# Kernel tuning notes

Measured on AMD Instinct MI355X. Metric: run time of the kernel, lower is better.

The kernel has to match this reference:

```python
import jax, jax.numpy as jnp
import numpy as np

EPS = 1e-5
HEADS = 4
DIM_HEAD = 64


def setup_inputs() -> dict:
    key = jax.random.key(0)
    k1, k2, k3, k4, k5, k6 = jax.random.split(key, 6)
    B, C, T, H, W = 2, 128, 40, 8, 8
    inner = HEADS * DIM_HEAD  # 256
    x = jax.random.normal(k1, (B, C, T, H, W), dtype=jnp.float32)
    g = jnp.ones((1, C, 1, 1, 1), dtype=jnp.float32) + 0.1 * jax.random.normal(k2, (1, C, 1, 1, 1), dtype=jnp.float32)
    b = 0.1 * jax.random.normal(k3, (1, C, 1, 1, 1), dtype=jnp.float32)
    w_qkv = 0.02 * jax.random.normal(k4, (inner * 3, C), dtype=jnp.float32)  # Conv1d(dim, inner*3, 1) weight squeezed
    w_out = 0.02 * jax.random.normal(k5, (C, inner), dtype=jnp.float32)      # Conv1d(inner, dim, 1) weight squeezed
    b_out = 0.02 * jax.random.normal(k6, (C,), dtype=jnp.float32)
    return {"x": x, "g": g, "b": b, "w_qkv": w_qkv, "w_out": w_out, "b_out": b_out}


def reference(x, g, b, w_qkv, w_out, b_out):
    B, C, T, H, W = x.shape
    n = T * H * W
    scale = DIM_HEAD ** -0.5
    # channel LayerNorm (var over dim=1, unbiased=False)
    mean = jnp.mean(x, axis=1, keepdims=True)
    std = jnp.sqrt(jnp.var(x, axis=1, keepdims=True))
    xn = (x - mean) / (std + EPS) * g + b
    xf = xn.reshape(B, C, n)  # b c n
    # 1x1 conv == matmul over channels
    qkv = jnp.einsum('oc,bcn->bon', w_qkv, xf)
    q, k, v = jnp.split(qkv, 3, axis=1)  # each [B, heads*d, n]
    def to_heads(t):  # b (h d) n -> b h n d
        return t.reshape(B, HEADS, DIM_HEAD, n).transpose(0, 1, 3, 2)
    q, k, v = to_heads(q) * scale, to_heads(k), to_heads(v)
    sim = jnp.einsum('bhid,bhjd->bhij', q, k)
    attn = jax.nn.softmax(sim, axis=-1)
    out = jnp.einsum('bhij,bhjd->bhid', attn, v)
    out = out.transpose(0, 1, 3, 2).reshape(B, HEADS * DIM_HEAD, n)  # b (h d) n
    out = jnp.einsum('oc,bcn->bon', w_out, out) + b_out[None, :, None]
    return out.reshape(B, C, T, H, W)
```

## Files before the change

kernel.cpp:

```cpp
#include <hip/hip_runtime.h>
#include <hip/hip_bf16.h>

#define HEADS 4
#define DHEAD 64
#define CC 128
#define NPOS 2560
#define NB 2
#define NSPLIT 4
#define NT_SPLIT ((NPOS / 64) / NSPLIT)

#define XN_ELE  ((size_t)NB * NPOS * CC)
#define QKV_ELE ((size_t)NB * HEADS * NPOS * DHEAD)
#define WS_BASE_BYTES  ((XN_ELE + 4 * QKV_ELE) * 2)
#define WS_SPLIT_BYTES ((XN_ELE + (4 + NSPLIT) * QKV_ELE) * 2 \
                        + (size_t)NSPLIT * NB * HEADS * NPOS * 8)

typedef __attribute__((ext_vector_type(8))) short short8;
typedef __attribute__((ext_vector_type(4))) short short4_t;
typedef __attribute__((ext_vector_type(4))) float f32x4;

#define SIDX(row, col) (((row) << 6) + ((col) ^ (((row) & 7) << 3)))

static __device__ __forceinline__ float b2f(short u) {
    union { unsigned int i; float f; } v;
    v.i = ((unsigned int)(unsigned short)u) << 16;
    return v.f;
}
static __device__ __forceinline__ short f2b(float f) {
    __hip_bfloat16 h = __float2bfloat16(f);
    union { __hip_bfloat16 h; unsigned short u; } v; v.h = h;
    return (short)v.u;
}

__global__ __launch_bounds__(256) void ln_kernel(
    const float* __restrict__ x, const float* __restrict__ g,
    const float* __restrict__ bb, short* __restrict__ xn) {
    int p0 = blockIdx.x * 64, b = blockIdx.y;
    __shared__ float tile[128][65];
    __shared__ float redsum[4][64], redsq[4][64], meanS[64], invS[64];
    int t = threadIdx.x, p = t & 63, cpart = t >> 6;
    float s = 0.f, sq = 0.f;
    for (int k = 0; k < 32; k++) {
        int c = cpart * 32 + k;
        float v = x[((b * CC + c) * NPOS) + p0 + p];
        tile[c][p] = v;
        s += v; sq += v * v;
    }
    redsum[cpart][p] = s; redsq[cpart][p] = sq;
    __syncthreads();
    if (t < 64) {
        float S = redsum[0][t] + redsum[1][t] + redsum[2][t] + redsum[3][t];
        float Q = redsq[0][t] + redsq[1][t] + redsq[2][t] + redsq[3][t];
        float mean = S * (1.f / CC);
        float var = fmaxf(Q * (1.f / CC) - mean * mean, 0.f);
        meanS[t] = mean;
        invS[t] = 1.f / (sqrtf(var) + 1e-5f);
    }
    __syncthreads();
    for (int k = 0; k < 32; k++) {
        int idx = k * 256 + t;
        int c = idx & 127, pp = idx >> 7;
        float v = (tile[c][pp] - meanS[pp]) * invS[pp] * g[c] + bb[c];
        xn[((size_t)(b * NPOS) + p0 + pp) * CC + c] = f2b(v);
    }
}

__global__ __launch_bounds__(256) void qkv_kernel(
    const float* __restrict__ w, const short* __restrict__ xn,
    short* __restrict__ q_ws, short* __restrict__ k_ws, short* __restrict__ v_ws) {
    int pt = blockIdx.x, ot = blockIdx.y, b = blockIdx.z;
    int p0 = pt * 64, o0 = ot * 64;
    __shared__ short Ws[64][136];
    __shared__ short Xs[64][136];
    int t = threadIdx.x, wv = t >> 6, l = t & 63;
    for (int i = 0; i < 8; i++) {
        int gidx = i * 256 + t;
        int r = gidx >> 5, cg = gidx & 31;
        f32x4 wv4 = *(const f32x4*)&w[(size_t)(o0 + r) * CC + cg * 4];
        short4_t sv = { f2b(wv4[0]), f2b(wv4[1]), f2b(wv4[2]), f2b(wv4[3]) };
        *(short4_t*)&Ws[r][cg * 4] = sv;
    }
    for (int i = 0; i < 4; i++) {
        int idx = i * 256 + t;
        int r = idx >> 4, ch = idx & 15;
        *(short8*)&Xs[r][ch * 8] = *(const short8*)&xn[((size_t)(b * NPOS) + p0 + r) * CC + ch * 8];
    }
    __syncthreads();
    f32x4 acc[4] = {{0,0,0,0},{0,0,0,0},{0,0,0,0},{0,0,0,0}};
    int lr = l & 15, lg = l >> 4;
    for (int kk = 0; kk < 4; kk++) {
        short8 a = *(short8*)&Ws[wv * 16 + lr][kk * 32 + lg * 8];
        for (int fb = 0; fb < 4; fb++) {
            short8 bf = *(short8*)&Xs[fb * 16 + lr][kk * 32 + lg * 8];
            acc[fb] = __builtin_amdgcn_mfma_f32_16x16x32_bf16(a, bf, acc[fb], 0, 0, 0);
        }
    }
    int orow0 = o0 + wv * 16 + lg * 4;
    int sec = orow0 >> 8;
    int oi = orow0 & 255, h = oi >> 6, d0 = oi & 63;
    size_t bh = (size_t)(b * HEADS + h);
    for (int fb = 0; fb < 4; fb++) {
        int pos = p0 + fb * 16 + lr;
        if (sec == 0) {
            short4_t qv = { f2b(acc[fb][0] * 0.125f), f2b(acc[fb][1] * 0.125f),
                            f2b(acc[fb][2] * 0.125f), f2b(acc[fb][3] * 0.125f) };
            *(short4_t*)&q_ws[(bh * NPOS + pos) * DHEAD + d0] = qv;
        } else if (sec == 1) {
            short4_t kv = { f2b(acc[fb][0]), f2b(acc[fb][1]), f2b(acc[fb][2]), f2b(acc[fb][3]) };
            *(short4_t*)&k_ws[(bh * NPOS + pos) * DHEAD + d0] = kv;
        } else {
            for (int r = 0; r < 4; r++)
                v_ws[(bh * DHEAD + d0 + r) * NPOS + pos] = f2b(acc[fb][r]);
        }
    }
}

template <int NT>
static __device__ __forceinline__ void attn_core(
    const short* __restrict__ kbp, const short* __restrict__ vbp,
    const short8* qreg, int kt0,
    short* Ks0, short* Ks1, short* Vs0, short* Vs1, short* PsT,
    int t, float& m_, float& l_, f32x4* acc) {
    int wv = t >> 6, l = t & 63;
    int lr = l & 15, lg = l >> 4;
    int sr0 = t >> 3, sr1 = sr0 + 32, sc = (t & 7) * 8;
    int prow = wv * 16 + lr;
    short* KsA[2] = { Ks0, Ks1 };
    short* VsA[2] = { Vs0, Vs1 };

    {
        int koff = kt0 * 64;
        *(short8*)&KsA[0][SIDX(sr0, sc)] = *(const short8*)&kbp[(size_t)(koff + sr0) * DHEAD + sc];
        *(short8*)&KsA[0][SIDX(sr1, sc)] = *(const short8*)&kbp[(size_t)(koff + sr1) * DHEAD + sc];
        *(short8*)&VsA[0][SIDX(sr0, sc)] = *(const short8*)&vbp[(size_t)sr0 * NPOS + koff + sc];
        *(short8*)&VsA[0][SIDX(sr1, sc)] = *(const short8*)&vbp[(size_t)sr1 * NPOS + koff + sc];
    }
    __syncthreads();

    for (int it = 0; it < NT; it++) {
        int cur = it & 1;
        bool pf = (it + 1 < NT);
        short8 kr0, kr1, vr0, vr1;
        if (pf) {
            int koff = (kt0 + it + 1) * 64;
            kr0 = *(const short8*)&kbp[(size_t)(koff + sr0) * DHEAD + sc];
            kr1 = *(const short8*)&kbp[(size_t)(koff + sr1) * DHEAD + sc];
            vr0 = *(const short8*)&vbp[(size_t)sr0 * NPOS + koff + sc];
            vr1 = *(const short8*)&vbp[(size_t)sr1 * NPOS + koff + sc];
        }
        f32x4 sf[4] = {{0,0,0,0},{0,0,0,0},{0,0,0,0},{0,0,0,0}};
        #pragma unroll
        for (int kk = 0; kk < 2; kk++) {
            #pragma unroll
            for (int fb = 0; fb < 4; fb++) {
                short8 kb = *(short8*)&KsA[cur][SIDX(fb * 16 + lr, kk * 32 + lg * 8)];
                sf[fb] = __builtin_amdgcn_mfma_f32_16x16x32_bf16(kb, qreg[kk], sf[fb], 0, 0, 0);
            }
        }
        float m0 = fmaxf(fmaxf(sf[0][0], sf[0][1]), fmaxf(sf[0][2], sf[0][3]));
        float m1 = fmaxf(fmaxf(sf[1][0], sf[1][1]), fmaxf(sf[1][2], sf[1][3]));
        float m2 = fmaxf(fmaxf(sf[2][0], sf[2][1]), fmaxf(sf[2][2], sf[2][3]));
        float m3 = fmaxf(fmaxf(sf[3][0], sf[3][1]), fmaxf(sf[3][2], sf[3][3]));
        float mx = fmaxf(fmaxf(m0, m1), fmaxf(m2, m3));
        mx = fmaxf(mx, __shfl_xor(mx, 16, 64));
        mx = fmaxf(mx, __shfl_xor(mx, 32, 64));
        float nm = fmaxf(m_, mx);
        float alpha = __expf(m_ - nm);
        float ps[4][4];
        float rs = 0.f;
        #pragma unroll
        for (int fb = 0; fb < 4; fb++) {
            float s0 = __expf(sf[fb][0] - nm), s1 = __expf(sf[fb][1] - nm);
            float s2 = __expf(sf[fb][2] - nm), s3 = __expf(sf[fb][3] - nm);
            ps[fb][0] = s0; ps[fb][1] = s1; ps[fb][2] = s2; ps[fb][3] = s3;
            rs += (s0 + s1) + (s2 + s3);
        }
        rs += __shfl_xor(rs, 16, 64);
        rs += __shfl_xor(rs, 32, 64);
        l_ = l_ * alpha + rs;
        m_ = nm;
        #pragma unroll
        for (int db = 0; db < 4; db++) {
            acc[db][0] *= alpha; acc[db][1] *= alpha;
            acc[db][2] *= alpha; acc[db][3] *= alpha;
        }
        #pragma unroll
        for (int fb = 0; fb < 4; fb++) {
            short4_t pk = { f2b(ps[fb][0]), f2b(ps[fb][1]), f2b(ps[fb][2]), f2b(ps[fb][3]) };
            *(short4_t*)&PsT[SIDX(prow, fb * 16 + lg * 4)] = pk;
        }
        #pragma unroll
        for (int kk = 0; kk < 2; kk++) {
            short8 pb = *(short8*)&PsT[SIDX(prow, kk * 32 + lg * 8)];
            #pragma unroll
            for (int db = 0; db < 4; db++) {
                short8 va = *(short8*)&VsA[cur][SIDX(db * 16 + lr, kk * 32 + lg * 8)];
                acc[db] = __builtin_amdgcn_mfma_f32_16x16x32_bf16(va, pb, acc[db], 0, 0, 0);
            }
        }
        if (pf) {
            *(short8*)&KsA[cur ^ 1][SIDX(sr0, sc)] = kr0;
            *(short8*)&KsA[cur ^ 1][SIDX(sr1, sc)] = kr1;
            *(short8*)&VsA[cur ^ 1][SIDX(sr0, sc)] = vr0;
            *(short8*)&VsA[cur ^ 1][SIDX(sr1, sc)] = vr1;
        }
        __syncthreads();
    }
}

__global__ __launch_bounds__(256) void attn_kernel(
    const short* __restrict__ q_ws, const short* __restrict__ k_ws,
    const short* __restrict__ v_ws, short* __restrict__ o_ws) {
    int qt = blockIdx.x, bh = blockIdx.y;
    int q0 = qt * 64;
    __shared__ short Ks[2][64 * 64];
    __shared__ short Vs[2][64 * 64];
    __shared__ short PsT[64 * 64];
    int t = threadIdx.x, wv = t >> 6, l = t & 63;
    int lr = l & 15, lg = l >> 4;
    const short* kbp = k_ws + (size_t)bh * NPOS * DHEAD;
    const short* vbp = v_ws + (size_t)bh * DHEAD * NPOS;
    short8 qreg[2];
    for (int kk = 0; kk < 2; kk++)
        qreg[kk] = *(const short8*)&q_ws[((size_t)bh * NPOS + q0 + wv * 16 + lr) * DHEAD + kk * 32 + lg * 8];
    float m_ = -1e9f, l_ = 0.f;
    f32x4 acc[4] = {{0,0,0,0},{0,0,0,0},{0,0,0,0},{0,0,0,0}};
    attn_core<NPOS / 64>(kbp, vbp, qreg, 0, Ks[0], Ks[1], Vs[0], Vs[1], PsT, t, m_, l_, acc);
    int h = bh & (HEADS - 1), b = bh >> 2;
    float inv = 1.f / l_;
    int pos = q0 + wv * 16 + lr;
    #pragma unroll
    for (int db = 0; db < 4; db++) {
        short4_t ov = { f2b(acc[db][0] * inv), f2b(acc[db][1] * inv),
                        f2b(acc[db][2] * inv), f2b(acc[db][3] * inv) };
        *(short4_t*)&o_ws[((size_t)(b * NPOS) + pos) * 256 + h * DHEAD + db * 16 + lg * 4] = ov;
    }
}

__global__ __launch_bounds__(256) void attn_split_kernel(
    const short* __restrict__ q_ws, const short* __restrict__ k_ws,
    const short* __restrict__ v_ws, short* __restrict__ po, float* __restrict__ ml) {
    int qt = blockIdx.x, bh = blockIdx.y, s = blockIdx.z;
    int q0 = qt * 64;
    __shared__ short Ks[2][64 * 64];
    __shared__ short Vs[2][64 * 64];
    __shared__ short PsT[64 * 64];
    int t = threadIdx.x, wv = t >> 6, l = t & 63;
    int lr = l & 15, lg = l >> 4;
    const short* kbp = k_ws + (size_t)bh * NPOS * DHEAD;
    const short* vbp = v_ws + (size_t)bh * DHEAD * NPOS;
    short8 qreg[2];
    for (int kk = 0; kk < 2; kk++)
        qreg[kk] = *(const short8*)&q_ws[((size_t)bh * NPOS + q0 + wv * 16 + lr) * DHEAD + kk * 32 + lg * 8];
    float m_ = -1e9f, l_ = 0.f;
    f32x4 acc[4] = {{0,0,0,0},{0,0,0,0},{0,0,0,0},{0,0,0,0}};
    attn_core<NT_SPLIT>(kbp, vbp, qreg, s * NT_SPLIT, Ks[0], Ks[1], Vs[0], Vs[1], PsT, t, m_, l_, acc);
    float inv = 1.f / l_;
    int pos = q0 + wv * 16 + lr;
    size_t sb = (size_t)(s * NB * HEADS + bh);
    #pragma unroll
    for (int db = 0; db < 4; db++) {
        short4_t ov = { f2b(acc[db][0] * inv), f2b(acc[db][1] * inv),
                        f2b(acc[db][2] * inv), f2b(acc[db][3] * inv) };
        *(short4_t*)&po[(sb * NPOS + pos) * DHEAD + db * 16 + lg * 4] = ov;
    }
    if (lg == 0) {
        ml[2 * (sb * NPOS + pos) + 0] = m_;
        ml[2 * (sb * NPOS + pos) + 1] = l_;
    }
}

__global__ __launch_bounds__(256) void combine_kernel(
    const short* __restrict__ po, const float* __restrict__ ml, short* __restrict__ o_ws) {
    int tid = blockIdx.x * 256 + threadIdx.x;
    int c8 = tid & 31;
    int posb = tid >> 5;
    int b = posb / NPOS, pos = posb - b * NPOS;
    int h = c8 >> 3, d0 = (c8 & 7) * 8;
    int bh = b * HEADS + h;
    float ms[NSPLIT], ls[NSPLIT], m = -1e30f;
    #pragma unroll
    for (int s = 0; s < NSPLIT; s++) {
        size_t sb = (size_t)(s * NB * HEADS + bh);
        ms[s] = ml[2 * (sb * NPOS + pos) + 0];
        ls[s] = ml[2 * (sb * NPOS + pos) + 1];
        m = fmaxf(m, ms[s]);
    }
    float w[NSPLIT], wsum = 0.f;
    #pragma unroll
    for (int s = 0; s < NSPLIT; s++) { w[s] = ls[s] * __expf(ms[s] - m); wsum += w[s]; }
    float o8[8] = {0,0,0,0,0,0,0,0};
    #pragma unroll
    for (int s = 0; s < NSPLIT; s++) {
        size_t sb = (size_t)(s * NB * HEADS + bh);
        short8 v = *(const short8*)&po[(sb * NPOS + pos) * DHEAD + d0];
        #pragma unroll
        for (int j = 0; j < 8; j++) o8[j] += w[s] * b2f(v[j]);
    }
    float inv = 1.f / wsum;
    short8 ov;
    #pragma unroll
    for (int j = 0; j < 8; j++) ov[j] = f2b(o8[j] * inv);
    *(short8*)&o_ws[((size_t)posb) * 256 + h * DHEAD + d0] = ov;
}

__global__ __launch_bounds__(256) void proj_kernel(
    const float* __restrict__ w_out, const float* __restrict__ b_out,
    const short* __restrict__ o_ws, float* __restrict__ out) {
    int pt = blockIdx.x, ct = blockIdx.y, b = blockIdx.z;
    int p0 = pt * 64, c0 = ct * 64;
    __shared__ short Ws[64][264];
    __shared__ short Os[64][264];
    int t = threadIdx.x, wv = t >> 6, l = t & 63;
    int lr = l & 15, lg = l >> 4;
    for (int i = 0; i < 16; i++) {
        int gidx = i * 256 + t;
        int r = gidx >> 6, cg = gidx & 63;
        f32x4 wv4 = *(const f32x4*)&w_out[(size_t)(c0 + r) * 256 + cg * 4];
        short4_t sv = { f2b(wv4[0]), f2b(wv4[1]), f2b(wv4[2]), f2b(wv4[3]) };
        *(short4_t*)&Ws[r][cg * 4] = sv;
    }
    for (int i = 0; i < 8; i++) {
        int gidx = i * 256 + t;
        int r = gidx >> 5, ch = gidx & 31;
        *(short8*)&Os[r][ch * 8] = *(const short8*)&o_ws[((size_t)(b * NPOS) + p0 + r) * 256 + ch * 8];
    }
    __syncthreads();
    f32x4 acc[4] = {{0,0,0,0},{0,0,0,0},{0,0,0,0},{0,0,0,0}};
    for (int kc = 0; kc < 8; kc++) {
        short8 a = *(short8*)&Ws[wv * 16 + lr][kc * 32 + lg * 8];
        #pragma unroll
        for (int fb = 0; fb < 4; fb++) {
            short8 ob = *(short8*)&Os[fb * 16 + lr][kc * 32 + lg * 8];
            acc[fb] = __builtin_amdgcn_mfma_f32_16x16x32_bf16(a, ob, acc[fb], 0, 0, 0);
        }
    }
    for (int r = 0; r < 4; r++) {
        int c = c0 + wv * 16 + lg * 4 + r;
        float bias = b_out[c];
        for (int fb = 0; fb < 4; fb++) {
            float vv = acc[fb][r] + bias;
            out[((size_t)(b * CC) + c) * NPOS + p0 + fb * 16 + lr] = vv;
        }
    }
}

extern "C" void kernel_launch(void* const* d_in, const int* in_sizes, int n_in,
                              void* d_out, int out_size, void* d_ws, size_t ws_size,
                              hipStream_t stream) {
    const float* x     = (const float*)d_in[0];
    const float* g     = (const float*)d_in[1];
    const float* b     = (const float*)d_in[2];
    const float* w_qkv = (const float*)d_in[3];
    const float* w_out = (const float*)d_in[4];
    const float* b_out = (const float*)d_in[5];
    float* out = (float*)d_out;

    const size_t out_bytes = (size_t)out_size * sizeof(float);

    {
        const int exp_sizes[6] = {655360, 128, 128, 98304, 32768, 128};
        int bad = -1;
        if (n_in != 6) bad = 15;
        else for (int i = 0; i < 6; i++) if (in_sizes[i] != exp_sizes[i]) { bad = i; break; }
        if (bad >= 0) { hipMemsetAsync(d_out, 0x50 | bad, out_bytes, stream); return; }
    }
    if (ws_size < WS_BASE_BYTES) {
        int mb = (int)(ws_size >> 20); if (mb > 15) mb = 15;
        hipMemsetAsync(d_out, 0x40 | mb, out_bytes, stream);
        return;
    }

    short* xn   = (short*)d_ws;
    short* q_ws = xn + XN_ELE;
    short* k_ws = q_ws + QKV_ELE;
    short* v_ws = k_ws + QKV_ELE;
    short* o_ws = v_ws + QKV_ELE;
    short* po   = o_ws + QKV_ELE;
    float* ml   = (float*)(po + NSPLIT * QKV_ELE);

    const bool use_split = (ws_size >= WS_SPLIT_BYTES);

    (void)hipGetLastError();
    ln_kernel<<<dim3(NPOS / 64, NB), 256, 0, stream>>>(x, g, b, xn);
    qkv_kernel<<<dim3(NPOS / 64, 12, NB), 256, 0, stream>>>(w_qkv, xn, q_ws, k_ws, v_ws);
    if (use_split) {
        attn_split_kernel<<<dim3(NPOS / 64, NB * HEADS, NSPLIT), 256, 0, stream>>>(q_ws, k_ws, v_ws, po, ml);
        combine_kernel<<<dim3(NB * NPOS * 32 / 256), 256, 0, stream>>>(po, ml, o_ws);
    } else {
        attn_kernel<<<dim3(NPOS / 64, NB * HEADS), 256, 0, stream>>>(q_ws, k_ws, v_ws, o_ws);
    }
    proj_kernel<<<dim3(NPOS / 64, 2, NB), 256, 0, stream>>>(w_out, b_out, o_ws, out);
    if (hipGetLastError() != hipSuccess) {
        hipMemsetAsync(d_out, 0xF0, out_bytes, stream);
    }
}
```

Measured before the change: 129.7 us.

## Fuse split-combine into projection, add lazy softmax rescale, single-buffer K/V

Removes the separate combine kernel and merges the split-KV reduction into the output projection's load stage, saving one launch and a round trip of the combined output through global memory. The softmax update now rescales the accumulators only when the running max rises by more than a threshold for some lane in the wave, which skips most alpha multiplies. K/V shared tiles go from double to single buffering, with an extra barrier around the refill. That cuts LDS use but serialises the tile store against compute. The proj blocks duplicate combine work across the two channel tiles.

```diff
diff --git a/kernel.cpp b/kernel.cpp
--- a/kernel.cpp
+++ b/kernel.cpp
@@ -119,26 +119,23 @@
 static __device__ __forceinline__ void attn_core(
     const short* __restrict__ kbp, const short* __restrict__ vbp,
     const short8* qreg, int kt0,
-    short* Ks0, short* Ks1, short* Vs0, short* Vs1, short* PsT,
+    short* Ks, short* Vs, short* PsT,
     int t, float& m_, float& l_, f32x4* acc) {
     int wv = t >> 6, l = t & 63;
     int lr = l & 15, lg = l >> 4;
     int sr0 = t >> 3, sr1 = sr0 + 32, sc = (t & 7) * 8;
     int prow = wv * 16 + lr;
-    short* KsA[2] = { Ks0, Ks1 };
-    short* VsA[2] = { Vs0, Vs1 };
 
     {
         int koff = kt0 * 64;
-        *(short8*)&KsA[0][SIDX(sr0, sc)] = *(const short8*)&kbp[(size_t)(koff + sr0) * DHEAD + sc];
-        *(short8*)&KsA[0][SIDX(sr1, sc)] = *(const short8*)&kbp[(size_t)(koff + sr1) * DHEAD + sc];
-        *(short8*)&VsA[0][SIDX(sr0, sc)] = *(const short8*)&vbp[(size_t)sr0 * NPOS + koff + sc];
-        *(short8*)&VsA[0][SIDX(sr1, sc)] = *(const short8*)&vbp[(size_t)sr1 * NPOS + koff + sc];
+        *(short8*)&Ks[SIDX(sr0, sc)] = *(const short8*)&kbp[(size_t)(koff + sr0) * DHEAD + sc];
+        *(short8*)&Ks[SIDX(sr1, sc)] = *(const short8*)&kbp[(size_t)(koff + sr1) * DHEAD + sc];
+        *(short8*)&Vs[SIDX(sr0, sc)] = *(const short8*)&vbp[(size_t)sr0 * NPOS + koff + sc];
+        *(short8*)&Vs[SIDX(sr1, sc)] = *(const short8*)&vbp[(size_t)sr1 * NPOS + koff + sc];
     }
     __syncthreads();
 
     for (int it = 0; it < NT; it++) {
-        int cur = it & 1;
         bool pf = (it + 1 < NT);
         short8 kr0, kr1, vr0, vr1;
         if (pf) {
@@ -153,7 +150,7 @@
         for (int kk = 0; kk < 2; kk++) {
             #pragma unroll
             for (int fb = 0; fb < 4; fb++) {
-                short8 kb = *(short8*)&KsA[cur][SIDX(fb * 16 + lr, kk * 32 + lg * 8)];
+                short8 kb = *(short8*)&Ks[SIDX(fb * 16 + lr, kk * 32 + lg * 8)];
                 sf[fb] = __builtin_amdgcn_mfma_f32_16x16x32_bf16(kb, qreg[kk], sf[fb], 0, 0, 0);
             }
         }
@@ -164,26 +161,29 @@
         float mx = fmaxf(fmaxf(m0, m1), fmaxf(m2, m3));
         mx = fmaxf(mx, __shfl_xor(mx, 16, 64));
         mx = fmaxf(mx, __shfl_xor(mx, 32, 64));
-        float nm = fmaxf(m_, mx);
-        float alpha = __expf(m_ - nm);
+        if (!__all(mx - m_ <= 8.0f)) {
+            float nm = fmaxf(m_, mx);
+            float alpha = __expf(m_ - nm);
+            l_ *= alpha;
+            #pragma unroll
+            for (int db = 0; db < 4; db++) {
+                acc[db][0] *= alpha; acc[db][1] *= alpha;
+                acc[db][2] *= alpha; acc[db][3] *= alpha;
+            }
+            m_ = nm;
+        }
         float ps[4][4];
         float rs = 0.f;
         #pragma unroll
         for (int fb = 0; fb < 4; fb++) {
-            float s0 = __expf(sf[fb][0] - nm), s1 = __expf(sf[fb][1] - nm);
-            float s2 = __expf(sf[fb][2] - nm), s3 = __expf(sf[fb][3] - nm);
+            float s0 = __expf(sf[fb][0] - m_), s1 = __expf(sf[fb][1] - m_);
+            float s2 = __expf(sf[fb][2] - m_), s3 = __expf(sf[fb][3] - m_);
             ps[fb][0] = s0; ps[fb][1] = s1; ps[fb][2] = s2; ps[fb][3] = s3;
             rs += (s0 + s1) + (s2 + s3);
         }
         rs += __shfl_xor(rs, 16, 64);
         rs += __shfl_xor(rs, 32, 64);
-        l_ = l_ * alpha + rs;
-        m_ = nm;
-        #pragma unroll
-        for (int db = 0; db < 4; db++) {
-            acc[db][0] *= alpha; acc[db][1] *= alpha;
-            acc[db][2] *= alpha; acc[db][3] *= alpha;
-        }
+        l_ += rs;
         #pragma unroll
         for (int fb = 0; fb < 4; fb++) {
             short4_t pk = { f2b(ps[fb][0]), f2b(ps[fb][1]), f2b(ps[fb][2]), f2b(ps[fb][3]) };
@@ -194,17 +194,18 @@
             short8 pb = *(short8*)&PsT[SIDX(prow, kk * 32 + lg * 8)];
             #pragma unroll
             for (int db = 0; db < 4; db++) {
-                short8 va = *(short8*)&VsA[cur][SIDX(db * 16 + lr, kk * 32 + lg * 8)];
+                short8 va = *(short8*)&Vs[SIDX(db * 16 + lr, kk * 32 + lg * 8)];
                 acc[db] = __builtin_amdgcn_mfma_f32_16x16x32_bf16(va, pb, acc[db], 0, 0, 0);
             }
         }
         if (pf) {
-            *(short8*)&KsA[cur ^ 1][SIDX(sr0, sc)] = kr0;
-            *(short8*)&KsA[cur ^ 1][SIDX(sr1, sc)] = kr1;
-            *(short8*)&VsA[cur ^ 1][SIDX(sr0, sc)] = vr0;
-            *(short8*)&VsA[cur ^ 1][SIDX(sr1, sc)] = vr1;
-        }
-        __syncthreads();
+            __syncthreads();
+            *(short8*)&Ks[SIDX(sr0, sc)] = kr0;
+            *(short8*)&Ks[SIDX(sr1, sc)] = kr1;
+            *(short8*)&Vs[SIDX(sr0, sc)] = vr0;
+            *(short8*)&Vs[SIDX(sr1, sc)] = vr1;
+            __syncthreads();
+        }
     }
 }
 
@@ -213,8 +214,8 @@
     const short* __restrict__ v_ws, short* __restrict__ o_ws) {
     int qt = blockIdx.x, bh = blockIdx.y;
     int q0 = qt * 64;
-    __shared__ short Ks[2][64 * 64];
-    __shared__ short Vs[2][64 * 64];
+    __shared__ short Ks[64 * 64];
+    __shared__ short Vs[64 * 64];
     __shared__ short PsT[64 * 64];
     int t = threadIdx.x, wv = t >> 6, l = t & 63;
     int lr = l & 15, lg = l >> 4;
@@ -225,7 +226,7 @@
         qreg[kk] = *(const short8*)&q_ws[((size_t)bh * NPOS + q0 + wv * 16 + lr) * DHEAD + kk * 32 + lg * 8];
     float m_ = -1e9f, l_ = 0.f;
     f32x4 acc[4] = {{0,0,0,0},{0,0,0,0},{0,0,0,0},{0,0,0,0}};
-    attn_core<NPOS / 64>(kbp, vbp, qreg, 0, Ks[0], Ks[1], Vs[0], Vs[1], PsT, t, m_, l_, acc);
+    attn_core<NPOS / 64>(kbp, vbp, qreg, 0, Ks, Vs, PsT, t, m_, l_, acc);
     int h = bh & (HEADS - 1), b = bh >> 2;
     float inv = 1.f / l_;
     int pos = q0 + wv * 16 + lr;
@@ -242,8 +243,8 @@
     const short* __restrict__ v_ws, short* __restrict__ po, float* __restrict__ ml) {
     int qt = blockIdx.x, bh = blockIdx.y, s = blockIdx.z;
     int q0 = qt * 64;
-    __shared__ short Ks[2][64 * 64];
-    __shared__ short Vs[2][64 * 64];
+    __shared__ short Ks[64 * 64];
+    __shared__ short Vs[64 * 64];
     __shared__ short PsT[64 * 64];
     int t = threadIdx.x, wv = t >> 6, l = t & 63;
     int lr = l & 15, lg = l >> 4;
@@ -254,7 +255,7 @@
         qreg[kk] = *(const short8*)&q_ws[((size_t)bh * NPOS + q0 + wv * 16 + lr) * DHEAD + kk * 32 + lg * 8];
     float m_ = -1e9f, l_ = 0.f;
     f32x4 acc[4] = {{0,0,0,0},{0,0,0,0},{0,0,0,0},{0,0,0,0}};
-    attn_core<NT_SPLIT>(kbp, vbp, qreg, s * NT_SPLIT, Ks[0], Ks[1], Vs[0], Vs[1], PsT, t, m_, l_, acc);
+    attn_core<NT_SPLIT>(kbp, vbp, qreg, s * NT_SPLIT, Ks, Vs, PsT, t, m_, l_, acc);
     float inv = 1.f / l_;
     int pos = q0 + wv * 16 + lr;
     size_t sb = (size_t)(s * NB * HEADS + bh);
@@ -270,43 +271,11 @@
     }
 }
 
-__global__ __launch_bounds__(256) void combine_kernel(
-    const short* __restrict__ po, const float* __restrict__ ml, short* __restrict__ o_ws) {
-    int tid = blockIdx.x * 256 + threadIdx.x;
-    int c8 = tid & 31;
-    int posb = tid >> 5;
-    int b = posb / NPOS, pos = posb - b * NPOS;
-    int h = c8 >> 3, d0 = (c8 & 7) * 8;
-    int bh = b * HEADS + h;
-    float ms[NSPLIT], ls[NSPLIT], m = -1e30f;
-    #pragma unroll
-    for (int s = 0; s < NSPLIT; s++) {
-        size_t sb = (size_t)(s * NB * HEADS + bh);
-        ms[s] = ml[2 * (sb * NPOS + pos) + 0];
-        ls[s] = ml[2 * (sb * NPOS + pos) + 1];
-        m = fmaxf(m, ms[s]);
-    }
-    float w[NSPLIT], wsum = 0.f;
-    #pragma unroll
-    for (int s = 0; s < NSPLIT; s++) { w[s] = ls[s] * __expf(ms[s] - m); wsum += w[s]; }
-    float o8[8] = {0,0,0,0,0,0,0,0};
-    #pragma unroll
-    for (int s = 0; s < NSPLIT; s++) {
-        size_t sb = (size_t)(s * NB * HEADS + bh);
-        short8 v = *(const short8*)&po[(sb * NPOS + pos) * DHEAD + d0];
-        #pragma unroll
-        for (int j = 0; j < 8; j++) o8[j] += w[s] * b2f(v[j]);
-    }
-    float inv = 1.f / wsum;
-    short8 ov;
-    #pragma unroll
-    for (int j = 0; j < 8; j++) ov[j] = f2b(o8[j] * inv);
-    *(short8*)&o_ws[((size_t)posb) * 256 + h * DHEAD + d0] = ov;
-}
-
+template <bool SPLIT>
 __global__ __launch_bounds__(256) void proj_kernel(
     const float* __restrict__ w_out, const float* __restrict__ b_out,
-    const short* __restrict__ o_ws, float* __restrict__ out) {
+    const short* __restrict__ o_ws, const short* __restrict__ po,
+    const float* __restrict__ ml, float* __restrict__ out) {
     int pt = blockIdx.x, ct = blockIdx.y, b = blockIdx.z;
     int p0 = pt * 64, c0 = ct * 64;
     __shared__ short Ws[64][264];
@@ -323,7 +292,37 @@
     for (int i = 0; i < 8; i++) {
         int gidx = i * 256 + t;
         int r = gidx >> 5, ch = gidx & 31;
-        *(short8*)&Os[r][ch * 8] = *(const short8*)&o_ws[((size_t)(b * NPOS) + p0 + r) * 256 + ch * 8];
+        if constexpr (SPLIT) {
+            int pos = p0 + r;
+            int h = ch >> 3, d0 = (ch & 7) * 8;
+            int bh = b * HEADS + h;
+            float ms[NSPLIT], ls[NSPLIT], m = -1e30f;
+            #pragma unroll
+            for (int s = 0; s < NSPLIT; s++) {
+                size_t sb = (size_t)(s * NB * HEADS + bh);
+                ms[s] = ml[2 * (sb * NPOS + pos) + 0];
+                ls[s] = ml[2 * (sb * NPOS + pos) + 1];
+                m = fmaxf(m, ms[s]);
+            }
+            float w4[NSPLIT], wsum = 0.f;
+            #pragma unroll
+            for (int s = 0; s < NSPLIT; s++) { w4[s] = ls[s] * __expf(ms[s] - m); wsum += w4[s]; }
+            float o8[8] = {0,0,0,0,0,0,0,0};
+            #pragma unroll
+            for (int s = 0; s < NSPLIT; s++) {
+                size_t sb = (size_t)(s * NB * HEADS + bh);
+                short8 v = *(const short8*)&po[(sb * NPOS + pos) * DHEAD + d0];
+                #pragma unroll
+                for (int j = 0; j < 8; j++) o8[j] += w4[s] * b2f(v[j]);
+            }
+            float invw = 1.f / wsum;
+            short8 ov;
+            #pragma unroll
+            for (int j = 0; j < 8; j++) ov[j] = f2b(o8[j] * invw);
+            *(short8*)&Os[r][ch * 8] = ov;
+        } else {
+            *(short8*)&Os[r][ch * 8] = *(const short8*)&o_ws[((size_t)(b * NPOS) + p0 + r) * 256 + ch * 8];
+        }
     }
     __syncthreads();
     f32x4 acc[4] = {{0,0,0,0},{0,0,0,0},{0,0,0,0},{0,0,0,0}};
@@ -386,11 +385,11 @@
     qkv_kernel<<<dim3(NPOS / 64, 12, NB), 256, 0, stream>>>(w_qkv, xn, q_ws, k_ws, v_ws);
     if (use_split) {
         attn_split_kernel<<<dim3(NPOS / 64, NB * HEADS, NSPLIT), 256, 0, stream>>>(q_ws, k_ws, v_ws, po, ml);
-        combine_kernel<<<dim3(NB * NPOS * 32 / 256), 256, 0, stream>>>(po, ml, o_ws);
+        proj_kernel<true><<<dim3(NPOS / 64, 2, NB), 256, 0, stream>>>(w_out, b_out, o_ws, po, ml, out);
     } else {
         attn_kernel<<<dim3(NPOS / 64, NB * HEADS), 256, 0, stream>>>(q_ws, k_ws, v_ws, o_ws);
-    }
-    proj_kernel<<<dim3(NPOS / 64, 2, NB), 256, 0, stream>>>(w_out, b_out, o_ws, out);
+        proj_kernel<false><<<dim3(NPOS / 64, 2, NB), 256, 0, stream>>>(w_out, b_out, o_ws, po, ml, out);
+    }
     if (hipGetLastError() != hipSuccess) {
         hipMemsetAsync(d_out, 0xF0, out_bytes, stream);
     }
```

New measurement: 111.8 us. 13.8% less time.
